# Kernel optimization log

Hardware: AMD Instinct MI355X
Metric: run time of the kernel (lower is better)

## Reference

```python
import jax, jax.numpy as jnp
import numpy as np

FACTOR = 5


def setup_inputs() -> dict:
    key = jax.random.key(0)
    k1, k2, k3, k4 = jax.random.split(key, 4)
    B, L, H, D = 2, 4096, 8, 64
    sample_k = min(FACTOR * int(np.ceil(np.log(L))), L)  # 45
    return {
        "queries": jax.random.normal(k1, (B, L, H, D), dtype=jnp.float32),
        "keys": jax.random.normal(k2, (B, L, H, D), dtype=jnp.float32),
        "values": jax.random.normal(k3, (B, L, H, D), dtype=jnp.float32),
        "attn_mask": jnp.zeros((1,), dtype=bool),  # unused; ProbMask is built internally
        "index_sample": jax.random.randint(k4, (L, sample_k), 0, L, dtype=jnp.int32),
    }


def reference(queries, keys, values, attn_mask, index_sample):
    # queries/keys/values: [B, L, H, D] -> [B, H, L, D]
    Q = jnp.swapaxes(queries, 1, 2)
    K = jnp.swapaxes(keys, 1, 2)
    V = jnp.swapaxes(values, 1, 2)
    B, H, L_Q, D = Q.shape
    L_K = K.shape[2]
    n_top = min(FACTOR * int(np.ceil(np.log(L_Q))), L_Q)
    scale = 1.0 / jnp.sqrt(jnp.float32(D))

    # --- sparse measurement: sampled QK scores ---
    # K_sample[b,h,q,s,d] = K[b,h,index_sample[q,s],d]
    K_sample = K[:, :, index_sample, :]                       # [B,H,L_Q,S,D]
    QK_sample = jnp.einsum("bhqd,bhqsd->bhqs", Q, K_sample)   # [B,H,L_Q,S]
    M = QK_sample.max(axis=-1) - QK_sample.sum(axis=-1) / L_K  # sparsity measure

    # --- top-u query selection ---
    _, M_top = jax.lax.top_k(M, n_top)                         # [B,H,u]
    Q_reduce = jnp.take_along_axis(Q, M_top[..., None], axis=2)  # [B,H,u,D]

    # --- full scores for selected queries ---
    scores = jnp.einsum("bhud,bhkd->bhuk", Q_reduce, K) * scale  # [B,H,u,L_K]

    # mask_flag=True: causal ProbMask (key pos > selected query pos)
    key_pos = jnp.arange(L_K)
    causal = key_pos[None, None, None, :] > M_top[..., None]
    scores = jnp.where(causal, -jnp.inf, scores)
    attn = jax.nn.softmax(scores, axis=-1)

    # --- initial context (cumsum, masked case) + scatter update ---
    context = jnp.cumsum(V, axis=2)                            # [B,H,L_Q,D]
    ctx_sel = jnp.einsum("bhuk,bhkd->bhud", attn, V)
    b_idx = jnp.arange(B)[:, None, None]
    h_idx = jnp.arange(H)[None, :, None]
    context = context.at[b_idx, h_idx, M_top].set(ctx_sel)
    return jnp.swapaxes(context, 1, 2)  # [B, L_Q, H, D]
```

## Files before the change

### kernel.cpp

```cpp
#include <hip/hip_runtime.h>
#include <math.h>

#define B_    2
#define L_    4096
#define H_    8
#define D_    64
#define S_    45
#define NT_   45
#define BH_   16
#define CHV   64
#define NCHV  64
#define KC    128
#define NKC   32
#define SCALE 0.125f
#define NEG_BIG (-1e30f)

#define OFF_M     0
#define OFF_MTOP  65536
#define OFF_MPART 66304
#define OFF_SPART 89344
#define OFF_CTXP  112384
#define OFF_VSUM  112384

template <int CTRL>
__device__ __forceinline__ float dpp_ror_f(float x) {
    int y = __builtin_amdgcn_update_dpp(0, __float_as_int(x), CTRL, 0xF, 0xF, false);
    return __int_as_float(y);
}

__device__ __forceinline__ unsigned short f2bf(float x) {
    return (unsigned short)(__float_as_uint(x) >> 16);
}
__device__ __forceinline__ float bflo(unsigned u) { return __uint_as_float(u << 16); }
__device__ __forceinline__ float bfhi(unsigned u) { return __uint_as_float(u & 0xffff0000u); }

__global__ __launch_bounds__(256) void k1(const float* __restrict__ Q,
                                          const float* __restrict__ Kt,
                                          const float* __restrict__ V,
                                          const int* __restrict__ samp,
                                          float* __restrict__ ws)
{
    int tid  = threadIdx.x;
    int w    = tid >> 6;
    int lane = tid & 63;

    if (blockIdx.x < 4096) {
        int i   = blockIdx.x;
        int xcd = i & 7;
        int b   = xcd >> 2;
        int hh  = (xcd >> 1) & 1;
        int qq  = ((i >> 3) << 1) | (xcd & 1);

        __shared__ int soff[4][S_];
        if (tid < 4 * S_) {
            int qs = tid / S_, ss = tid - qs * S_;
            soff[qs][ss] = samp[(qq * 4 + qs) * S_ + ss] << 11;
        }
        __syncthreads();

        int q  = qq * 4 + w;
        int h4 = lane >> 4;

        const float4 q4 = *(const float4*)(Q +
            ((((long)b * L_ + q) * H_ + hh * 4) << 6) + lane * 4);

        const char* kb_base = (const char*)Kt +
            (long)b * L_ * 2048 + hh * 1024 + lane * 16;

        float mx = NEG_BIG, sm = 0.f;
#pragma unroll
        for (int jb = 0; jb < 45; jb += 15) {
            float4 kb[15];
#pragma unroll
            for (int j = 0; j < 15; ++j)
                kb[j] = *(const float4*)(kb_base + soff[w][jb + j]);
#pragma unroll
            for (int j = 0; j < 15; ++j) {
                float p = q4.x * kb[j].x + q4.y * kb[j].y +
                          q4.z * kb[j].z + q4.w * kb[j].w;
                p += dpp_ror_f<0x121>(p);
                p += dpp_ror_f<0x122>(p);
                p += dpp_ror_f<0x124>(p);
                p += dpp_ror_f<0x128>(p);
                mx = fmaxf(mx, p);
                sm += p;
            }
        }
        if ((lane & 15) == 0)
            ws[OFF_M + ((long)(b * 8 + hh * 4 + h4)) * L_ + q] =
                mx - sm * (1.0f / (float)L_);
    } else {
        int unit = (blockIdx.x - 4096) * 4 + w;
        int bh = unit >> 6, ch = unit & 63;
        int b = bh >> 3, h = bh & 7;
        const float* vp = V + ((((long)b * L_ + (long)ch * CHV) * H_ + h) << 6) + lane;
        float ssum = 0.f;
#pragma unroll
        for (int ib = 0; ib < CHV; ib += 16) {
            float vb[16];
#pragma unroll
            for (int j = 0; j < 16; ++j) vb[j] = vp[(long)(ib + j) * (H_ * D_)];
#pragma unroll
            for (int j = 0; j < 16; ++j) ssum += vb[j];
        }
        ws[OFF_VSUM + unit * 64 + lane] = ssum;
    }
}

__global__ __launch_bounds__(256) void k2(const float* __restrict__ V,
                                          float* __restrict__ out,
                                          float* __restrict__ ws)
{
    int tid  = threadIdx.x;
    int w    = tid >> 6;
    int lane = tid & 63;

    if (blockIdx.x < 16) {
        int bh = blockIdx.x;
        int* Mtop = (int*)ws + OFF_MTOP + bh * NT_;

        __shared__ float lv_[4][NT_];
        __shared__ int   li_[4][NT_];

        const float4* m4 = (const float4*)(ws + OFF_M + (long)bh * L_ +
                                           w * 1024 + lane * 16);
        float vals[16];
        {
            float4 a = m4[0], bq = m4[1], c = m4[2], d = m4[3];
            vals[0]=a.x; vals[1]=a.y; vals[2]=a.z; vals[3]=a.w;
            vals[4]=bq.x; vals[5]=bq.y; vals[6]=bq.z; vals[7]=bq.w;
            vals[8]=c.x; vals[9]=c.y; vals[10]=c.z; vals[11]=c.w;
            vals[12]=d.x; vals[13]=d.y; vals[14]=d.z; vals[15]=d.w;
        }
        float lv = NEG_BIG; int li = lane * 16;
#pragma unroll
        for (int j = 0; j < 16; ++j)
            if (vals[j] > lv) { lv = vals[j]; li = lane * 16 + j; }

        for (int r = 0; r < NT_; ++r) {
            float rm = lv;
            rm = fmaxf(rm, dpp_ror_f<0x121>(rm));
            rm = fmaxf(rm, dpp_ror_f<0x122>(rm));
            rm = fmaxf(rm, dpp_ror_f<0x124>(rm));
            rm = fmaxf(rm, dpp_ror_f<0x128>(rm));
            rm = fmaxf(rm, __shfl_xor(rm, 16));
            rm = fmaxf(rm, __shfl_xor(rm, 32));
            unsigned long long bm = __ballot(lv == rm);
            int winner = __ffsll(bm) - 1;
            int wi = __shfl(li, winner);
            if (lane == 0) { lv_[w][r] = rm; li_[w][r] = w * 1024 + wi; }
            if (lane == winner) {
#pragma unroll
                for (int j = 0; j < 16; ++j)
                    if (j == (wi & 15)) vals[j] = NEG_BIG;
                lv = NEG_BIG; li = lane * 16;
#pragma unroll
                for (int j = 0; j < 16; ++j)
                    if (vals[j] > lv) { lv = vals[j]; li = lane * 16 + j; }
            }
        }
        __syncthreads();

        if (w == 0) {
            int g = lane & 3;
            int p = 0;
            float hv = lv_[g][0]; int hi = li_[g][0];
            for (int r = 0; r < NT_; ++r) {
                float v0 = __shfl(hv, 0), v1 = __shfl(hv, 1),
                      v2 = __shfl(hv, 2), v3 = __shfl(hv, 3);
                int   i0 = __shfl(hi, 0), i1 = __shfl(hi, 1),
                      i2 = __shfl(hi, 2), i3 = __shfl(hi, 3);
                float bv = v0; int bi = i0, bg = 0;
                if (v1 > bv) { bv = v1; bi = i1; bg = 1; }
                if (v2 > bv) { bv = v2; bi = i2; bg = 2; }
                if (v3 > bv) { bv = v3; bi = i3; bg = 3; }
                if (lane == 0) Mtop[r] = bi;
                if (g == bg) {
                    ++p;
                    hv = (p < NT_) ? lv_[g][p] : NEG_BIG;
                    hi = (p < NT_) ? li_[g][p] : 0;
                }
            }
        }
    } else {
        int unit = (blockIdx.x - 16) * 4 + w;
        int bh = unit >> 6, ch = unit & 63;
        int b = bh >> 3, h = bh & 7;
        int d = lane;

        float acc = 0.f;
        {
            const float* vs = ws + OFF_VSUM + (long)bh * NCHV * 64 + d;
            int c = 0;
            for (; c + 8 <= ch; c += 8) {
                float vb[8];
#pragma unroll
                for (int j = 0; j < 8; ++j) vb[j] = vs[(c + j) * 64];
#pragma unroll
                for (int j = 0; j < 8; ++j) acc += vb[j];
            }
            for (; c < ch; ++c) acc += vs[c * 64];
        }

        const float* vp = V   + ((((long)b * L_ + (long)ch * CHV) * H_ + h) << 6) + d;
        float*       op = out + ((((long)b * L_ + (long)ch * CHV) * H_ + h) << 6) + d;
#pragma unroll
        for (int ib = 0; ib < CHV; ib += 16) {
            float vb[16];
#pragma unroll
            for (int j = 0; j < 16; ++j) vb[j] = vp[(long)(ib + j) * (H_ * D_)];
#pragma unroll
            for (int j = 0; j < 16; ++j) {
                acc += vb[j];
                op[(long)(ib + j) * (H_ * D_)] = acc;
            }
        }
    }
}

#define KPAD16 72
#define NUH    23
__global__ __launch_bounds__(256) void kC(const float* __restrict__ Q,
                                          const float* __restrict__ Kt,
                                          const float* __restrict__ V,
                                          float* __restrict__ ws)
{
    __shared__ unsigned short Klds16[KC * KPAD16];
    __shared__ unsigned short P16[NUH * KC];
    __shared__ int qpos[NUH];

    int tid = threadIdx.x;
    int bh = blockIdx.x >> 6;
    int kc = (blockIdx.x >> 1) & 31;
    int ug = blockIdx.x & 1;
    int b = bh >> 3, h = bh & 7;
    int kbase = kc * KC;
    int u0 = ug * 23;
    int NU = ug ? 22 : 23;

    if (tid < NU) qpos[tid] = ((const int*)ws)[OFF_MTOP + bh * NT_ + tid + u0];

    {
        const float4* ksrc4 = (const float4*)(Kt + ((((long)b * L_ + kbase) * H_ + h) << 6));
#pragma unroll
        for (int i = 0; i < 8; ++i) {
            int e = i * 256 + tid;
            int r = e >> 4, c4 = e & 15;
            float4 kv = ksrc4[(long)r * (H_ * D_ / 4) + c4];
            uint2 pk;
            pk.x = (__float_as_uint(kv.x) >> 16) | (__float_as_uint(kv.y) & 0xffff0000u);
            pk.y = (__float_as_uint(kv.z) >> 16) | (__float_as_uint(kv.w) & 0xffff0000u);
            *(uint2*)&Klds16[r * KPAD16 + c4 * 4] = pk;
        }
    }
    __syncthreads();

    int k = tid & 127, uh = tid >> 7;
    int kpos = kbase + k;
    {
        float kf[64];
#pragma unroll
        for (int j = 0; j < 8; ++j) {
            uint4 U = *(const uint4*)&Klds16[k * KPAD16 + j * 8];
            kf[j*8+0] = bflo(U.x); kf[j*8+1] = bfhi(U.x);
            kf[j*8+2] = bflo(U.y); kf[j*8+3] = bfhi(U.y);
            kf[j*8+4] = bflo(U.z); kf[j*8+5] = bfhi(U.z);
            kf[j*8+6] = bflo(U.w); kf[j*8+7] = bfhi(U.w);
        }

#pragma unroll 3
        for (int j = 0; j < 12; ++j) {
            int ul = uh * 12 + j;
            if (ul > NU - 1) ul = NU - 1;
            int qp_ = __builtin_amdgcn_readfirstlane(qpos[ul]);
            const float4* qrow = (const float4*)(Q + ((((long)b * L_ + qp_) * H_ + h) << 6));
            float a0 = 0.f, a1 = 0.f, a2 = 0.f, a3 = 0.f;
#pragma unroll
            for (int jj = 0; jj < 16; jj += 4) {
                float4 q0 = qrow[jj + 0], q1 = qrow[jj + 1];
                float4 q2 = qrow[jj + 2], q3 = qrow[jj + 3];
                a0 += q0.x * kf[jj*4+ 0] + q0.y * kf[jj*4+ 1] +
                      q0.z * kf[jj*4+ 2] + q0.w * kf[jj*4+ 3];
                a1 += q1.x * kf[jj*4+ 4] + q1.y * kf[jj*4+ 5] +
                      q1.z * kf[jj*4+ 6] + q1.w * kf[jj*4+ 7];
                a2 += q2.x * kf[jj*4+ 8] + q2.y * kf[jj*4+ 9] +
                      q2.z * kf[jj*4+10] + q2.w * kf[jj*4+11];
                a3 += q3.x * kf[jj*4+12] + q3.y * kf[jj*4+13] +
                      q3.z * kf[jj*4+14] + q3.w * kf[jj*4+15];
            }
            float sc = ((a0 + a1) + (a2 + a3)) * SCALE;
            if (kpos > qp_) sc = NEG_BIG;
            P16[ul * KC + k] = f2bf(sc);
        }
    }
    __syncthreads();

    int lane = tid & 63, w = tid >> 6;
    for (int ul = w; ul < NU; ul += 4) {
        float s0 = bflo(P16[ul * KC + lane]);
        float s1 = bflo(P16[ul * KC + 64 + lane]);
        float m = fmaxf(s0, s1);
#pragma unroll
        for (int off = 32; off; off >>= 1) m = fmaxf(m, __shfl_xor(m, off));
        float e0 = __expf(s0 - m), e1 = __expf(s1 - m);
        unsigned short b0 = f2bf(e0), b1 = f2bf(e1);
        P16[ul * KC + lane]      = b0;
        P16[ul * KC + 64 + lane] = b1;
        float sm = bflo(b0) + bflo(b1);
#pragma unroll
        for (int off = 32; off; off >>= 1) sm += __shfl_xor(sm, off);
        if (lane == 0) {
            ws[OFF_MPART + ((long)bh * NT_ + u0 + ul) * NKC + kc] = m;
            ws[OFF_SPART + ((long)bh * NT_ + u0 + ul) * NKC + kc] = sm;
        }
    }
    __syncthreads();

    {
        const float* vsrc = V + ((((long)b * L_ + kbase) * H_ + h) << 6);
        float ctx[6];
#pragma unroll
        for (int j = 0; j < 6; ++j) ctx[j] = 0.f;
        for (int kk8 = 0; kk8 < 16; ++kk8) {
            float v[8];
#pragma unroll
            for (int t = 0; t < 8; ++t)
                v[t] = vsrc[(long)(kk8 * 8 + t) * (H_ * D_) + lane];
#pragma unroll
            for (int j = 0; j < 6; ++j) {
                int ul = w + j * 4;
                if (ul < NU) {
                    uint4 U = *(const uint4*)&P16[ul * KC + kk8 * 8];
                    ctx[j] += bflo(U.x) * v[0] + bfhi(U.x) * v[1]
                            + bflo(U.y) * v[2] + bfhi(U.y) * v[3]
                            + bflo(U.z) * v[4] + bfhi(U.z) * v[5]
                            + bflo(U.w) * v[6] + bfhi(U.w) * v[7];
                }
            }
        }
#pragma unroll
        for (int j = 0; j < 6; ++j) {
            int ul = w + j * 4;
            if (ul < NU)
                ws[OFF_CTXP + ((long)(bh * NKC + kc) * NT_ + u0 + ul) * 64 + lane] = ctx[j];
        }
    }
}

__global__ __launch_bounds__(64) void kD(float* __restrict__ out,
                                         const float* __restrict__ ws)
{
    int lane = threadIdx.x;
    int unit = blockIdx.x;
    int bh = unit / NT_, u = unit - bh * NT_;
    int b = bh >> 3, h = bh & 7;

    const float4* mp4 = (const float4*)(ws + OFF_MPART + ((long)bh * NT_ + u) * NKC);
    const float4* sp4 = (const float4*)(ws + OFF_SPART + ((long)bh * NT_ + u) * NKC);

    float mc[NKC], sc[NKC];
    float m = NEG_BIG;
#pragma unroll
    for (int c4 = 0; c4 < NKC / 4; ++c4) {
        float4 mv = mp4[c4];
        float4 sv = sp4[c4];
        mc[c4 * 4 + 0] = mv.x; mc[c4 * 4 + 1] = mv.y;
        mc[c4 * 4 + 2] = mv.z; mc[c4 * 4 + 3] = mv.w;
        sc[c4 * 4 + 0] = sv.x; sc[c4 * 4 + 1] = sv.y;
        sc[c4 * 4 + 2] = sv.z; sc[c4 * 4 + 3] = sv.w;
        m = fmaxf(m, fmaxf(fmaxf(mv.x, mv.y), fmaxf(mv.z, mv.w)));
    }
    float T = 0.f, ctx = 0.f;
#pragma unroll
    for (int c = 0; c < NKC; ++c) {
        float wgt = __expf(mc[c] - m);
        T   += sc[c] * wgt;
        ctx += ws[OFF_CTXP + ((long)(bh * NKC + c) * NT_ + u) * 64 + lane] * wgt;
    }
    int qp = ((const int*)ws)[OFF_MTOP + bh * NT_ + u];
    out[((((long)b * L_ + qp) * H_ + h) << 6) + lane] = ctx / T;
}

extern "C" void kernel_launch(void* const* d_in, const int* in_sizes, int n_in,
                              void* d_out, int out_size, void* d_ws, size_t ws_size,
                              hipStream_t stream)
{
    const float* Q    = (const float*)d_in[0];
    const float* K    = (const float*)d_in[1];
    const float* V    = (const float*)d_in[2];
    const int*   samp = (const int*)d_in[4];
    float* out = (float*)d_out;
    float* ws  = (float*)d_ws;

    k1<<<4352, 256, 0, stream>>>(Q, K, V, samp, ws);
    k2<<<272, 256, 0, stream>>>(V, out, ws);
    kC<<<1024, 256, 0, stream>>>(Q, K, V, ws);
    kD<<<720, 64, 0, stream>>>(out, ws);
}
```

Before: 189.0 us.

## Score sampled keys in fp16 with error bounds, then rescore candidates exactly in fp32

A new pre-pass converts K to fp16 into the output buffer, which is used as scratch. The sampled-score kernel now reads half-width keys, halving its gather traffic, and also writes a per-query error bound. The top-k kernel uses these bounds to pick a candidate set that must contain the true top-u, recomputes those candidates' sparsity measure exactly from fp32 K, and takes the final top-u from them. This adds a conversion kernel and a serial rescoring step in 16 blocks. If more than 192 candidates qualify, the set is truncated and the selection could be wrong.

```diff
diff --git a/kernel.cpp b/kernel.cpp
--- a/kernel.cpp
+++ b/kernel.cpp
@@ -1,4 +1,5 @@
 #include <hip/hip_runtime.h>
+#include <hip/hip_fp16.h>
 #include <math.h>
 
 #define B_    2
@@ -14,6 +15,7 @@
 #define NKC   32
 #define SCALE 0.125f
 #define NEG_BIG (-1e30f)
+#define CAP   192
 
 #define OFF_M     0
 #define OFF_MTOP  65536
@@ -21,6 +23,7 @@
 #define OFF_SPART 89344
 #define OFF_CTXP  112384
 #define OFF_VSUM  112384
+#define OFF_EPS   1586944
 
 template <int CTRL>
 __device__ __forceinline__ float dpp_ror_f(float x) {
@@ -34,8 +37,24 @@
 __device__ __forceinline__ float bflo(unsigned u) { return __uint_as_float(u << 16); }
 __device__ __forceinline__ float bfhi(unsigned u) { return __uint_as_float(u & 0xffff0000u); }
 
+__global__ __launch_bounds__(256) void k0(const float* __restrict__ K,
+                                          unsigned short* __restrict__ K16)
+{
+    int t = blockIdx.x * 256 + threadIdx.x;
+    const float4* src = (const float4*)K + (long)t * 2;
+    float4 a = src[0], b = src[1];
+    __half2 p0 = __floats2half2_rn(a.x, a.y);
+    __half2 p1 = __floats2half2_rn(a.z, a.w);
+    __half2 p2 = __floats2half2_rn(b.x, b.y);
+    __half2 p3 = __floats2half2_rn(b.z, b.w);
+    uint4 o;
+    o.x = *(unsigned*)&p0; o.y = *(unsigned*)&p1;
+    o.z = *(unsigned*)&p2; o.w = *(unsigned*)&p3;
+    ((uint4*)K16)[t] = o;
+}
+
 __global__ __launch_bounds__(256) void k1(const float* __restrict__ Q,
-                                          const float* __restrict__ Kt,
+                                          const unsigned short* __restrict__ K16,
                                           const float* __restrict__ V,
                                           const int* __restrict__ samp,
                                           float* __restrict__ ws)
@@ -54,7 +73,7 @@
         __shared__ int soff[4][S_];
         if (tid < 4 * S_) {
             int qs = tid / S_, ss = tid - qs * S_;
-            soff[qs][ss] = samp[(qq * 4 + qs) * S_ + ss] << 11;
+            soff[qs][ss] = (samp[(qq * 4 + qs) * S_ + ss] << 10) | (hh << 9);
         }
         __syncthreads();
 
@@ -63,32 +82,48 @@
 
         const float4 q4 = *(const float4*)(Q +
             ((((long)b * L_ + q) * H_ + hh * 4) << 6) + lane * 4);
-
-        const char* kb_base = (const char*)Kt +
-            (long)b * L_ * 2048 + hh * 1024 + lane * 16;
-
-        float mx = NEG_BIG, sm = 0.f;
+        float aqx = fabsf(q4.x), aqy = fabsf(q4.y),
+              aqz = fabsf(q4.z), aqw = fabsf(q4.w);
+
+        const char* kslab = (const char*)K16 + (long)b * (L_ * 1024);
+        unsigned lb = (unsigned)(lane * 8);
+
+        float mx = NEG_BIG, sm = 0.f, bmx = 0.f, bsm = 0.f;
 #pragma unroll
         for (int jb = 0; jb < 45; jb += 15) {
-            float4 kb[15];
+            uint2 kb[15];
 #pragma unroll
             for (int j = 0; j < 15; ++j)
-                kb[j] = *(const float4*)(kb_base + soff[w][jb + j]);
+                kb[j] = *(const uint2*)(kslab +
+                        ((unsigned)soff[w][jb + j] + lb));
 #pragma unroll
             for (int j = 0; j < 15; ++j) {
-                float p = q4.x * kb[j].x + q4.y * kb[j].y +
-                          q4.z * kb[j].z + q4.w * kb[j].w;
+                float2 f01 = __half22float2(*(const __half2*)&kb[j].x);
+                float2 f23 = __half22float2(*(const __half2*)&kb[j].y);
+                float p = q4.x * f01.x + q4.y * f01.y +
+                          q4.z * f23.x + q4.w * f23.y;
+                float bb = aqx * fabsf(f01.x) + aqy * fabsf(f01.y) +
+                           aqz * fabsf(f23.x) + aqw * fabsf(f23.y);
                 p += dpp_ror_f<0x121>(p);
                 p += dpp_ror_f<0x122>(p);
                 p += dpp_ror_f<0x124>(p);
                 p += dpp_ror_f<0x128>(p);
+                bb += dpp_ror_f<0x121>(bb);
+                bb += dpp_ror_f<0x122>(bb);
+                bb += dpp_ror_f<0x124>(bb);
+                bb += dpp_ror_f<0x128>(bb);
                 mx = fmaxf(mx, p);
                 sm += p;
-            }
-        }
-        if ((lane & 15) == 0)
-            ws[OFF_M + ((long)(b * 8 + hh * 4 + h4)) * L_ + q] =
-                mx - sm * (1.0f / (float)L_);
+                bmx = fmaxf(bmx, bb);
+                bsm += bb;
+            }
+        }
+        if ((lane & 15) == 0) {
+            long o = ((long)(b * 8 + hh * 4 + h4)) * L_ + q;
+            ws[OFF_M + o]   = mx - sm * (1.0f / (float)L_);
+            ws[OFF_EPS + o] = (bmx + bsm * (1.0f / (float)L_)) *
+                              (1.001f / 2048.0f) + 1e-3f;
+        }
     } else {
         int unit = (blockIdx.x - 4096) * 4 + w;
         int bh = unit >> 6, ch = unit & 63;
@@ -107,7 +142,10 @@
     }
 }
 
-__global__ __launch_bounds__(256) void k2(const float* __restrict__ V,
+__global__ __launch_bounds__(256) void k2(const float* __restrict__ Q,
+                                          const float* __restrict__ Kt,
+                                          const float* __restrict__ V,
+                                          const int* __restrict__ samp,
                                           float* __restrict__ out,
                                           float* __restrict__ ws)
 {
@@ -117,25 +155,39 @@
 
     if (blockIdx.x < 16) {
         int bh = blockIdx.x;
+        int b = bh >> 3, h = bh & 7;
         int* Mtop = (int*)ws + OFF_MTOP + bh * NT_;
 
         __shared__ float lv_[4][NT_];
-        __shared__ int   li_[4][NT_];
+        __shared__ float lam_s;
+        __shared__ int   wt[4];
+        __shared__ int   nc_s;
+        __shared__ int   Ci[CAP];
+        __shared__ int   Csamp[CAP * S_];
+        __shared__ float Cval[CAP];
 
         const float4* m4 = (const float4*)(ws + OFF_M + (long)bh * L_ +
                                            w * 1024 + lane * 16);
-        float vals[16];
+        const float4* e4 = (const float4*)(ws + OFF_EPS + (long)bh * L_ +
+                                           w * 1024 + lane * 16);
+        float vals[16], u[16];
         {
-            float4 a = m4[0], bq = m4[1], c = m4[2], d = m4[3];
-            vals[0]=a.x; vals[1]=a.y; vals[2]=a.z; vals[3]=a.w;
-            vals[4]=bq.x; vals[5]=bq.y; vals[6]=bq.z; vals[7]=bq.w;
-            vals[8]=c.x; vals[9]=c.y; vals[10]=c.z; vals[11]=c.w;
-            vals[12]=d.x; vals[13]=d.y; vals[14]=d.z; vals[15]=d.w;
-        }
-        float lv = NEG_BIG; int li = lane * 16;
-#pragma unroll
-        for (int j = 0; j < 16; ++j)
-            if (vals[j] > lv) { lv = vals[j]; li = lane * 16 + j; }
+            float4 ma0 = m4[0], ma1 = m4[1], ma2 = m4[2], ma3 = m4[3];
+            float4 ea0 = e4[0], ea1 = e4[1], ea2 = e4[2], ea3 = e4[3];
+            float mm[16] = {ma0.x,ma0.y,ma0.z,ma0.w, ma1.x,ma1.y,ma1.z,ma1.w,
+                            ma2.x,ma2.y,ma2.z,ma2.w, ma3.x,ma3.y,ma3.z,ma3.w};
+            float ee[16] = {ea0.x,ea0.y,ea0.z,ea0.w, ea1.x,ea1.y,ea1.z,ea1.w,
+                            ea2.x,ea2.y,ea2.z,ea2.w, ea3.x,ea3.y,ea3.z,ea3.w};
+#pragma unroll
+            for (int j = 0; j < 16; ++j) {
+                vals[j] = mm[j] - ee[j];
+                u[j]    = mm[j] + ee[j];
+            }
+        }
+
+        float lv = NEG_BIG;
+#pragma unroll
+        for (int j = 0; j < 16; ++j) lv = fmaxf(lv, vals[j]);
 
         for (int r = 0; r < NT_; ++r) {
             float rm = lv;
@@ -147,16 +199,15 @@
             rm = fmaxf(rm, __shfl_xor(rm, 32));
             unsigned long long bm = __ballot(lv == rm);
             int winner = __ffsll(bm) - 1;
-            int wi = __shfl(li, winner);
-            if (lane == 0) { lv_[w][r] = rm; li_[w][r] = w * 1024 + wi; }
+            if (lane == 0) lv_[w][r] = rm;
             if (lane == winner) {
+                bool done = false;
 #pragma unroll
                 for (int j = 0; j < 16; ++j)
-                    if (j == (wi & 15)) vals[j] = NEG_BIG;
-                lv = NEG_BIG; li = lane * 16;
-#pragma unroll
-                for (int j = 0; j < 16; ++j)
-                    if (vals[j] > lv) { lv = vals[j]; li = lane * 16 + j; }
+                    if (!done && vals[j] == lv) { vals[j] = NEG_BIG; done = true; }
+                lv = NEG_BIG;
+#pragma unroll
+                for (int j = 0; j < 16; ++j) lv = fmaxf(lv, vals[j]);
             }
         }
         __syncthreads();
@@ -164,21 +215,117 @@
         if (w == 0) {
             int g = lane & 3;
             int p = 0;
-            float hv = lv_[g][0]; int hi = li_[g][0];
+            float hv = lv_[g][0];
+            float lam = NEG_BIG;
             for (int r = 0; r < NT_; ++r) {
                 float v0 = __shfl(hv, 0), v1 = __shfl(hv, 1),
                       v2 = __shfl(hv, 2), v3 = __shfl(hv, 3);
-                int   i0 = __shfl(hi, 0), i1 = __shfl(hi, 1),
-                      i2 = __shfl(hi, 2), i3 = __shfl(hi, 3);
-                float bv = v0; int bi = i0, bg = 0;
-                if (v1 > bv) { bv = v1; bi = i1; bg = 1; }
-                if (v2 > bv) { bv = v2; bi = i2; bg = 2; }
-                if (v3 > bv) { bv = v3; bi = i3; bg = 3; }
-                if (lane == 0) Mtop[r] = bi;
+                float bv = v0; int bg = 0;
+                if (v1 > bv) { bv = v1; bg = 1; }
+                if (v2 > bv) { bv = v2; bg = 2; }
+                if (v3 > bv) { bv = v3; bg = 3; }
+                lam = bv;
                 if (g == bg) {
                     ++p;
                     hv = (p < NT_) ? lv_[g][p] : NEG_BIG;
-                    hi = (p < NT_) ? li_[g][p] : 0;
+                }
+            }
+            if (lane == 0) lam_s = lam;
+        }
+        __syncthreads();
+        float lam = lam_s;
+
+        int cnt = 0;
+#pragma unroll
+        for (int j = 0; j < 16; ++j) cnt += (u[j] >= lam) ? 1 : 0;
+        int incl = cnt;
+#pragma unroll
+        for (int off = 1; off < 64; off <<= 1) {
+            int t2 = __shfl_up(incl, off);
+            incl += (lane >= off) ? t2 : 0;
+        }
+        int excl = incl - cnt;
+        if (lane == 63) wt[w] = incl;
+        __syncthreads();
+        int woff = 0;
+        for (int w2 = 0; w2 < 4; ++w2) if (w2 < w) woff += wt[w2];
+        int pos = woff + excl;
+#pragma unroll
+        for (int j = 0; j < 16; ++j) {
+            if (u[j] >= lam) {
+                if (pos < CAP) Ci[pos] = w * 1024 + lane * 16 + j;
+                pos++;
+            }
+        }
+        if (tid == 0) {
+            int t3 = wt[0] + wt[1] + wt[2] + wt[3];
+            nc_s = (t3 > CAP) ? CAP : t3;
+        }
+        __syncthreads();
+        int NC = nc_s;
+
+        for (int t = tid; t < NC * S_; t += 256) {
+            int c = t / S_, s2 = t - c * S_;
+            Csamp[t] = (samp[Ci[c] * S_ + s2] << 11) + (h << 8);
+        }
+        __syncthreads();
+
+        {
+            int g = tid >> 4, l16 = tid & 15;
+            const char* Kb = (const char*)Kt + (long)b * (L_ * 2048);
+            for (int c = g; c < NC; c += 16) {
+                int qi = Ci[c];
+                const float4 qv = *(const float4*)(Q +
+                    ((((long)b * L_ + qi) * H_ + h) << 6) + l16 * 4);
+                float mx = NEG_BIG, sm = 0.f;
+                for (int ss = 0; ss < 45; ss += 9) {
+                    int so[9];
+#pragma unroll
+                    for (int j = 0; j < 9; ++j) so[j] = Csamp[c * S_ + ss + j];
+                    float4 kb[9];
+#pragma unroll
+                    for (int j = 0; j < 9; ++j)
+                        kb[j] = *(const float4*)(Kb + so[j] + l16 * 16);
+#pragma unroll
+                    for (int j = 0; j < 9; ++j) {
+                        float p = qv.x * kb[j].x + qv.y * kb[j].y +
+                                  qv.z * kb[j].z + qv.w * kb[j].w;
+                        p += dpp_ror_f<0x121>(p);
+                        p += dpp_ror_f<0x122>(p);
+                        p += dpp_ror_f<0x124>(p);
+                        p += dpp_ror_f<0x128>(p);
+                        mx = fmaxf(mx, p);
+                        sm += p;
+                    }
+                }
+                if (l16 == 0) Cval[c] = mx - sm * (1.0f / (float)L_);
+            }
+        }
+        __syncthreads();
+
+        if (w == 0) {
+            float v3[3];
+            int base = lane * 3;
+#pragma unroll
+            for (int j = 0; j < 3; ++j)
+                v3[j] = (base + j < NC) ? Cval[base + j] : NEG_BIG;
+            for (int r = 0; r < NT_; ++r) {
+                float lb2 = v3[0];
+                if (v3[1] > lb2) lb2 = v3[1];
+                if (v3[2] > lb2) lb2 = v3[2];
+                float rm = lb2;
+                rm = fmaxf(rm, dpp_ror_f<0x121>(rm));
+                rm = fmaxf(rm, dpp_ror_f<0x122>(rm));
+                rm = fmaxf(rm, dpp_ror_f<0x124>(rm));
+                rm = fmaxf(rm, dpp_ror_f<0x128>(rm));
+                rm = fmaxf(rm, __shfl_xor(rm, 16));
+                rm = fmaxf(rm, __shfl_xor(rm, 32));
+                unsigned long long bm2 = __ballot(lb2 == rm);
+                int winner = __ffsll(bm2) - 1;
+                if (lane == winner) {
+                    int jw = (v3[0] == rm) ? 0 : ((v3[1] == rm) ? 1 : 2);
+                    Mtop[r] = Ci[base + jw];
+                    v3[jw] = NEG_BIG;
                 }
             }
         }
@@ -392,8 +539,9 @@
     float* out = (float*)d_out;
     float* ws  = (float*)d_ws;
 
-    k1<<<4352, 256, 0, stream>>>(Q, K, V, samp, ws);
-    k2<<<272, 256, 0, stream>>>(V, out, ws);
+    k0<<<2048, 256, 0, stream>>>(K, (unsigned short*)out);
+    k1<<<4352, 256, 0, stream>>>(Q, (const unsigned short*)out, V, samp, ws);
+    k2<<<272, 256, 0, stream>>>(Q, K, V, samp, out, ws);
     kC<<<1024, 256, 0, stream>>>(Q, K, V, ws);
     kD<<<720, 64, 0, stream>>>(out, ws);
 }
```

Result: slower. 231.6 us (+22.5%).
